# Optimization experiments

Hardware: AMD Instinct MI355X
Metric: run time of the kernel (lower is better)

The kernel has to match this reference:

```python
import jax, jax.numpy as jnp
import numpy as np

B, S, H, D = 4, 2048, 16, 64
DM = H * D  # d_model = 1024


def setup_inputs() -> dict:
    key = jax.random.key(0)
    ks = jax.random.split(key, 11)
    s = 1.0 / np.sqrt(DM)
    return {
        "query": jax.random.normal(ks[0], (B, S, DM), jnp.float32),
        "key": jax.random.normal(ks[1], (B, S, DM), jnp.float32),
        "value": jax.random.normal(ks[2], (B, S, DM), jnp.float32),
        "Wq": jax.random.uniform(ks[3], (DM, DM), jnp.float32, -s, s),
        "bq": jax.random.uniform(ks[4], (DM,), jnp.float32, -s, s),
        "Wk": jax.random.uniform(ks[5], (DM, DM), jnp.float32, -s, s),
        "bk": jax.random.uniform(ks[6], (DM,), jnp.float32, -s, s),
        "Wv": jax.random.uniform(ks[7], (DM, DM), jnp.float32, -s, s),
        "bv": jax.random.uniform(ks[8], (DM,), jnp.float32, -s, s),
        "Wo": jax.random.uniform(ks[9], (DM, DM), jnp.float32, -s, s),
        "bo": jax.random.uniform(ks[10], (DM,), jnp.float32, -s, s),
        "masking": 1,
    }


def reference(query, key, value, Wq, bq, Wk, bk, Wv, bv, Wo, bo, masking):
    b, s, _ = query.shape
    # Linear projections (torch Linear: x @ W.T + b), split into heads
    q = (query @ Wq.T + bq).reshape(b, s, H, D).transpose(0, 2, 1, 3)  # [B,H,S,D]
    k = (key @ Wk.T + bk).reshape(b, -1, H, D).transpose(0, 2, 1, 3)
    v = (value @ Wv.T + bv).reshape(b, -1, H, D).transpose(0, 2, 1, 3)
    scores = jnp.einsum("bhqd,bhkd->bhqk", q, k) / np.power(D, 0.5)
    if masking:
        # subsequent (strictly upper-triangular) mask -> fill with -1e9
        sub = jnp.triu(jnp.ones((s, k.shape[2]), bool), k=1)
        scores = jnp.where(sub, jnp.float32(-1e9), scores)
    attn = jax.nn.softmax(scores, axis=-1)
    out = jnp.einsum("bhqk,bhkd->bhqd", attn, v)  # [B,H,S,D]
    out = out.transpose(0, 2, 1, 3).reshape(b, s, H * D)
    return out @ Wo.T + bo
```

## Files before the change

kernel.cpp:

```cpp
#include <hip/hip_runtime.h>
#include <stdint.h>
#include <stddef.h>

#define B_ 4
#define S_ 2048
#define H_ 16
#define D_ 64
#define DM 1024
#define MTOT 8192
#define QSCALE 0.1803368867f

typedef __bf16 bf16x8 __attribute__((ext_vector_type(8)));
typedef __bf16 bf16x4 __attribute__((ext_vector_type(4)));
typedef float  f32x4  __attribute__((ext_vector_type(4)));

__device__ __forceinline__ void g2l16(const void* g, void* l) {
  __builtin_amdgcn_global_load_lds(
      (__attribute__((address_space(1))) void*)g,
      (__attribute__((address_space(3))) void*)l, 16, 0, 0);
}

__global__ __launch_bounds__(256) void cvt_kernel(const float* __restrict__ src,
                                                  __bf16* __restrict__ dst, int n4,
                                                  float scale) {
  int i = blockIdx.x * 256 + threadIdx.x;
  if (i < n4) {
    const float4 v = ((const float4*)src)[i];
    bf16x4 o;
    o.x = (__bf16)(v.x * scale); o.y = (__bf16)(v.y * scale);
    o.z = (__bf16)(v.z * scale); o.w = (__bf16)(v.w * scale);
    ((bf16x4*)dst)[i] = o;
  }
}

struct QKVArgs {
  const __bf16 *A0, *A1, *A2;
  const __bf16 *W0, *W1, *W2;
  const float *b0, *b1, *b2;
  __bf16 *oQ, *oK, *oVt;
};

__global__ __launch_bounds__(256) void gemm_qkv(QKVArgs args) {
  const int z = blockIdx.z;
  const __bf16* A    = (z == 0) ? args.A0 : (z == 1) ? args.A1 : args.A2;
  const __bf16* W    = (z == 0) ? args.W0 : (z == 1) ? args.W1 : args.W2;
  const float*  bias = (z == 0) ? args.b0 : (z == 1) ? args.b1 : args.b2;
  const float   bsc  = (z == 0) ? QSCALE : 1.0f;

  __shared__ __bf16 As[128 * 32];
  __shared__ __bf16 Bs[128 * 32];

  const int m0 = blockIdx.x * 128;
  const int n0 = blockIdx.y * 128;
  const int tid = threadIdx.x;
  const int wave = tid >> 6, lane = tid & 63;
  const int lrow = lane & 15, lhi = lane >> 4;
  const int moff = (wave & 1) * 64, noff = (wave >> 1) * 64;
  const int srow = lane >> 2;
  const int schunk = (lane & 3) * 8;

  f32x4 acc[4][4] = {};

  for (int k0 = 0; k0 < DM; k0 += 32) {
#pragma unroll
    for (int p = 0; p < 2; ++p) {
      const int rg = (p * 4 + wave) * 16;
      g2l16(A + (size_t)(m0 + rg + srow) * DM + k0 + schunk, As + rg * 32 + lane * 8);
      g2l16(W + (size_t)(n0 + rg + srow) * DM + k0 + schunk, Bs + rg * 32 + lane * 8);
    }
    __syncthreads();
    bf16x8 af[4], bfr[4];
#pragma unroll
    for (int i = 0; i < 4; ++i) {
      af[i]  = *(const bf16x8*)(As + (moff + i * 16 + lrow) * 32 + lhi * 8);
      bfr[i] = *(const bf16x8*)(Bs + (noff + i * 16 + lrow) * 32 + lhi * 8);
    }
#pragma unroll
    for (int i = 0; i < 4; ++i)
#pragma unroll
      for (int j = 0; j < 4; ++j)
        acc[i][j] = __builtin_amdgcn_mfma_f32_16x16x32_bf16(af[i], bfr[j], acc[i][j], 0, 0, 0);
    __syncthreads();
  }

  if (z < 2) {
    __bf16* out = (z == 0) ? args.oQ : args.oK;
#pragma unroll
    for (int i = 0; i < 4; ++i)
#pragma unroll
      for (int j = 0; j < 4; ++j)
#pragma unroll
        for (int r = 0; r < 4; ++r) {
          const int row = m0 + moff + i * 16 + lhi * 4 + r;
          const int col = n0 + noff + j * 16 + lrow;
          out[(size_t)row * DM + col] = (__bf16)(acc[i][j][r] + bias[col] * bsc);
        }
  } else {
    __bf16* out = args.oVt;
#pragma unroll
    for (int i = 0; i < 4; ++i)
#pragma unroll
      for (int j = 0; j < 4; ++j)
#pragma unroll
        for (int r = 0; r < 4; ++r) {
          const int row = m0 + moff + i * 16 + lhi * 4 + r;
          const int col = n0 + noff + j * 16 + lrow;
          const int bb = row >> 11, s = row & 2047;
          const int hh = col >> 6,  d = col & 63;
          out[(((size_t)(bb * H_ + hh) * D_ + d) << 11) + s] =
              (__bf16)(acc[i][j][r] + bias[col]);
        }
  }
}

__global__ __launch_bounds__(256) void gemm_oproj(const __bf16* __restrict__ A,
                                                  const __bf16* __restrict__ W,
                                                  const float* __restrict__ bias,
                                                  float* __restrict__ out) {
  __shared__ __bf16 As[128 * 32];
  __shared__ __bf16 Bs[128 * 32];

  const int m0 = blockIdx.x * 128;
  const int n0 = blockIdx.y * 128;
  const int tid = threadIdx.x;
  const int wave = tid >> 6, lane = tid & 63;
  const int lrow = lane & 15, lhi = lane >> 4;
  const int moff = (wave & 1) * 64, noff = (wave >> 1) * 64;
  const int srow = lane >> 2;
  const int schunk = (lane & 3) * 8;

  f32x4 acc[4][4] = {};

  for (int k0 = 0; k0 < DM; k0 += 32) {
#pragma unroll
    for (int p = 0; p < 2; ++p) {
      const int rg = (p * 4 + wave) * 16;
      g2l16(A + (size_t)(m0 + rg + srow) * DM + k0 + schunk, As + rg * 32 + lane * 8);
      g2l16(W + (size_t)(n0 + rg + srow) * DM + k0 + schunk, Bs + rg * 32 + lane * 8);
    }
    __syncthreads();
    bf16x8 af[4], bfr[4];
#pragma unroll
    for (int i = 0; i < 4; ++i) {
      af[i]  = *(const bf16x8*)(As + (moff + i * 16 + lrow) * 32 + lhi * 8);
      bfr[i] = *(const bf16x8*)(Bs + (noff + i * 16 + lrow) * 32 + lhi * 8);
    }
#pragma unroll
    for (int i = 0; i < 4; ++i)
#pragma unroll
      for (int j = 0; j < 4; ++j)
        acc[i][j] = __builtin_amdgcn_mfma_f32_16x16x32_bf16(af[i], bfr[j], acc[i][j], 0, 0, 0);
    __syncthreads();
  }

#pragma unroll
  for (int i = 0; i < 4; ++i)
#pragma unroll
    for (int j = 0; j < 4; ++j)
#pragma unroll
      for (int r = 0; r < 4; ++r) {
        const int row = m0 + moff + i * 16 + lhi * 4 + r;
        const int col = n0 + noff + j * 16 + lrow;
        out[(size_t)row * DM + col] = acc[i][j][r] + bias[col];
      }
}

__global__ __launch_bounds__(256, 3) void attn_kernel(const __bf16* __restrict__ Q,
                                                      const __bf16* __restrict__ K,
                                                      const __bf16* __restrict__ Vt,
                                                      __bf16* __restrict__ O) {
  const int id = blockIdx.x;
  const int slot = id >> 8;
  const int tau = id & 255;
  const int k4 = (tau >> 3) & 3;
  const int bh = ((tau >> 5) << 3) | (tau & 7);
  const int b = bh >> 4, h = bh & 15;

  int tiles[2];
  int ntile;
  if (slot == 0)      { ntile = 1; tiles[0] = 15 - k4; tiles[1] = 0; }
  else if (slot == 1) { ntile = 1; tiles[0] = 8 + k4;  tiles[1] = 0; }
  else                { ntile = 2; tiles[0] = k4;      tiles[1] = 7 - k4; }

  const int wave = threadIdx.x >> 6;
  const int lane = threadIdx.x & 63;
  const int lq = lane & 15, lhi = lane >> 4;

  const __bf16* Qb = Q + (size_t)b * S_ * DM + h * D_;
  const __bf16* Kb = K + (size_t)b * S_ * DM + h * D_;
  const __bf16* Vb = Vt + (size_t)bh * D_ * S_;

  __shared__ __bf16 Ks[2][64 * 64];
  __shared__ __bf16 Vs[2][64 * 64];
  __shared__ __bf16 Ps[4][32 * 72];
  __bf16* const Pw = Ps[wave];

  const int rl = lane >> 3;
  const int cg8 = ((lane & 7) ^ rl) * 8;

  for (int ti = 0; ti < ntile; ++ti) {
    const int t = tiles[ti];
    const int qw0 = t * 128 + wave * 32;
    const int jend = t * 128 + 64;

    if (ti) __syncthreads();

    bf16x8 qb[2][2];
#pragma unroll
    for (int m = 0; m < 2; ++m)
#pragma unroll
      for (int kd = 0; kd < 2; ++kd)
        qb[m][kd] = *(const bf16x8*)(Qb + (size_t)(qw0 + m * 16 + lq) * DM + kd * 32 + lhi * 8);

    f32x4 o_acc[2][4] = {};
    float rs[2] = {0.f, 0.f};

#pragma unroll
    for (int i = 0; i < 2; ++i) {
      const int row = wave * 16 + i * 8 + rl;
      g2l16(Kb + (size_t)row * DM + cg8, Ks[0] + ((wave * 16 + i * 8) << 6) + lane * 8);
      g2l16(Vb + (size_t)row * S_ + cg8, Vs[0] + ((wave * 16 + i * 8) << 6) + lane * 8);
    }

    int p = 0;
    for (int j0 = 0; j0 <= jend; j0 += 64) {
      __syncthreads();
      if (j0 < jend) {
        const int jn = j0 + 64;
#pragma unroll
        for (int i = 0; i < 2; ++i) {
          const int row = wave * 16 + i * 8 + rl;
          g2l16(Kb + (size_t)(jn + row) * DM + cg8, Ks[p ^ 1] + ((wave * 16 + i * 8) << 6) + lane * 8);
          g2l16(Vb + (size_t)row * S_ + jn + cg8, Vs[p ^ 1] + ((wave * 16 + i * 8) << 6) + lane * 8);
        }
      }

      bf16x8 kf[4][2];
#pragma unroll
      for (int kt = 0; kt < 4; ++kt) {
        const int r = kt * 16 + lq;
#pragma unroll
        for (int kd = 0; kd < 2; ++kd)
          kf[kt][kd] = *(const bf16x8*)(Ks[p] + (r << 6) + (((kd * 4 + lhi) ^ (r & 7)) << 3));
      }

      bf16x8 vf[4][2];
#pragma unroll
      for (int dt = 0; dt < 4; ++dt) {
        const int r = dt * 16 + lq;
#pragma unroll
        for (int kk = 0; kk < 2; ++kk)
          vf[dt][kk] = *(const bf16x8*)(Vs[p] + (r << 6) + (((kk * 4 + lhi) ^ (r & 7)) << 3));
      }

      f32x4 sc[2][4];
#pragma unroll
      for (int m = 0; m < 2; ++m)
#pragma unroll
        for (int kt = 0; kt < 4; ++kt) {
          f32x4 s = {};
          s = __builtin_amdgcn_mfma_f32_16x16x32_bf16(kf[kt][0], qb[m][0], s, 0, 0, 0);
          s = __builtin_amdgcn_mfma_f32_16x16x32_bf16(kf[kt][1], qb[m][1], s, 0, 0, 0);
          sc[m][kt] = s;
        }

#pragma unroll
      for (int m = 0; m < 2; ++m) {
        const bool dg = (j0 + 63 > qw0 + m * 16);
        const int thr = qw0 + m * 16 + lq - j0;
#pragma unroll
        for (int kt = 0; kt < 4; ++kt) {
          bf16x4 pk;
#pragma unroll
          for (int r = 0; r < 4; ++r) {
            float v = sc[m][kt][r];
            if (dg && (kt * 16 + lhi * 4 + r > thr)) v = -1e9f;
            const float pv = exp2f(v);
            rs[m] += pv;
            pk[r] = (__bf16)pv;
          }
          *(bf16x4*)(Pw + (m * 16 + lq) * 72 + kt * 16 + lhi * 4) = pk;
        }
      }

#pragma unroll
      for (int m = 0; m < 2; ++m) {
        bf16x8 pa[2];
#pragma unroll
        for (int kk = 0; kk < 2; ++kk)
          pa[kk] = *(const bf16x8*)(Pw + (m * 16 + lq) * 72 + kk * 32 + lhi * 8);
#pragma unroll
        for (int dt = 0; dt < 4; ++dt) {
          o_acc[m][dt] = __builtin_amdgcn_mfma_f32_16x16x32_bf16(pa[0], vf[dt][0], o_acc[m][dt], 0, 0, 0);
          o_acc[m][dt] = __builtin_amdgcn_mfma_f32_16x16x32_bf16(pa[1], vf[dt][1], o_acc[m][dt], 0, 0, 0);
        }
      }
      p ^= 1;
    }

#pragma unroll
    for (int m = 0; m < 2; ++m) {
      rs[m] += __shfl_xor(rs[m], 16);
      rs[m] += __shfl_xor(rs[m], 32);
    }

#pragma unroll
    for (int m = 0; m < 2; ++m)
#pragma unroll
      for (int r = 0; r < 4; ++r) {
        const float inv = 1.0f / __shfl(rs[m], lhi * 4 + r);
        const int qrow = qw0 + m * 16 + lhi * 4 + r;
        __bf16* orow = O + ((size_t)b * S_ + qrow) * DM + h * D_;
#pragma unroll
        for (int dt = 0; dt < 4; ++dt)
          orow[dt * 16 + lq] = (__bf16)(o_acc[m][dt][r] * inv);
      }
  }
}

extern "C" void kernel_launch(void* const* d_in, const int* in_sizes, int n_in,
                              void* d_out, int out_size, void* d_ws, size_t ws_size,
                              hipStream_t stream) {
  (void)in_sizes; (void)n_in; (void)out_size; (void)ws_size;
  const float* query = (const float*)d_in[0];
  const float* key   = (const float*)d_in[1];
  const float* value = (const float*)d_in[2];
  const float* Wq = (const float*)d_in[3];
  const float* bq = (const float*)d_in[4];
  const float* Wk = (const float*)d_in[5];
  const float* bk = (const float*)d_in[6];
  const float* Wv = (const float*)d_in[7];
  const float* bv = (const float*)d_in[8];
  const float* Wo = (const float*)d_in[9];
  const float* bo = (const float*)d_in[10];

  const size_t NX = (size_t)MTOT * DM;
  const size_t NW = (size_t)DM * DM;
  __bf16* p = (__bf16*)d_ws;
  __bf16 *Xq = p, *Xk = Xq + NX, *Xv = Xk + NX;
  __bf16 *Wqb = Xv + NX, *Wkb = Wqb + NW, *Wvb = Wkb + NW, *Wob = Wvb + NW;
  __bf16 *Qrm = Wob + NW, *Krm = Qrm + NX, *Vt = Krm + NX, *Orm = Vt + NX;

  const int nbx = (int)(NX / 4 / 256);
  const int nbw = (int)(NW / 4 / 256);
  cvt_kernel<<<nbx, 256, 0, stream>>>(query, Xq, (int)(NX / 4), 1.0f);
  cvt_kernel<<<nbx, 256, 0, stream>>>(key,   Xk, (int)(NX / 4), 1.0f);
  cvt_kernel<<<nbx, 256, 0, stream>>>(value, Xv, (int)(NX / 4), 1.0f);
  cvt_kernel<<<nbw, 256, 0, stream>>>(Wq, Wqb, (int)(NW / 4), QSCALE);
  cvt_kernel<<<nbw, 256, 0, stream>>>(Wk, Wkb, (int)(NW / 4), 1.0f);
  cvt_kernel<<<nbw, 256, 0, stream>>>(Wv, Wvb, (int)(NW / 4), 1.0f);
  cvt_kernel<<<nbw, 256, 0, stream>>>(Wo, Wob, (int)(NW / 4), 1.0f);

  QKVArgs qa;
  qa.A0 = Xq; qa.A1 = Xk; qa.A2 = Xv;
  qa.W0 = Wqb; qa.W1 = Wkb; qa.W2 = Wvb;
  qa.b0 = bq; qa.b1 = bk; qa.b2 = bv;
  qa.oQ = Qrm; qa.oK = Krm; qa.oVt = Vt;
  gemm_qkv<<<dim3(MTOT / 128, DM / 128, 3), 256, 0, stream>>>(qa);

  attn_kernel<<<dim3(768), 256, 0, stream>>>(Qrm, Krm, Vt, Orm);

  gemm_oproj<<<dim3(MTOT / 128, DM / 128), 256, 0, stream>>>(Orm, Wob, bo, (float*)d_out);
}
```

Before: 345.1 us.

## Pipeline GEMMs with triple-buffered swizzled LDS, 256x128 tiles, and fuse conversions

Replaces the simple single-buffer GEMM loop in the QKV and output projections with a shared main loop. It uses 256x128 tiles, a triple-buffered LDS ring filled by global_load_lds, XOR-swizzled LDS addressing to avoid bank conflicts, and MFMA phases interleaved with prefetches under raised wave priority. The aim is to hide global-load latency behind compute and raise data reuse per tile. The seven fp32-to-bf16 conversion launches are also merged into one launch to cut launch overhead. The cost is more registers and LDS per block (occupancy 2), plus hand-tuned waitcnt logic that is fragile.

```diff
diff --git a/kernel.cpp b/kernel.cpp
--- a/kernel.cpp
+++ b/kernel.cpp
@@ -20,17 +20,124 @@
       (__attribute__((address_space(3))) void*)l, 16, 0, 0);
 }
 
-__global__ __launch_bounds__(256) void cvt_kernel(const float* __restrict__ src,
-                                                  __bf16* __restrict__ dst, int n4,
-                                                  float scale) {
-  int i = blockIdx.x * 256 + threadIdx.x;
-  if (i < n4) {
-    const float4 v = ((const float4*)src)[i];
-    bf16x4 o;
-    o.x = (__bf16)(v.x * scale); o.y = (__bf16)(v.y * scale);
-    o.z = (__bf16)(v.z * scale); o.w = (__bf16)(v.w * scale);
-    ((bf16x4*)dst)[i] = o;
+struct Cvt7 {
+  const float* s[7];
+  __bf16* d[7];
+  float sc[7];
+};
+__global__ __launch_bounds__(256) void cvt_all(Cvt7 a) {
+  const int b = blockIdx.x;
+  int seg, i;
+  if (b < 24576) { seg = b >> 13; i = ((b & 8191) << 8) + threadIdx.x; }
+  else { const int sb = b - 24576; seg = 3 + (sb >> 10); i = ((sb & 1023) << 8) + threadIdx.x; }
+  const float sc = a.sc[seg];
+  const float4 v = ((const float4*)a.s[seg])[i];
+  bf16x4 o;
+  o.x = (__bf16)(v.x * sc); o.y = (__bf16)(v.y * sc);
+  o.z = (__bf16)(v.z * sc); o.w = (__bf16)(v.w * sc);
+  ((bf16x4*)a.d[seg])[i] = o;
+}
+
+__device__ __forceinline__ void gemm_main(const __bf16* __restrict__ A,
+                                          const __bf16* __restrict__ W,
+                                          int m0, int n0,
+                                          __bf16* ldsA, __bf16* ldsB,
+                                          f32x4 (&acc)[8][4]) {
+  const int tid = threadIdx.x;
+  const int lane = tid & 63, wave = tid >> 6;
+  const int lq = lane & 15, lhi = lane >> 4;
+  const int wr = wave >> 1, wc = wave & 1;
+
+  const int srow = tid >> 2;
+  const int cso = ((tid & 3) ^ (srow & 3)) * 8;
+  const __bf16* pA = A + (size_t)(m0 + srow) * DM + cso;
+  const __bf16* pB = W + (size_t)(n0 + srow) * DM + cso;
+  const int tid8 = tid * 8;
+
+  const int sx = (lhi ^ (lq & 3)) * 8;
+  const int aB = (wr * 128 + lq) * 32 + sx;
+  const int bB = (wc * 64 + lq) * 32 + sx;
+
+#define SA(q, ko, bs) g2l16(pA + (size_t)(q) * 64 * DM + (ko), ldsA + (bs) * 8192 + (q) * 2048 + tid8)
+#define SB(q, ko, bs) g2l16(pB + (size_t)(q) * 64 * DM + (ko), ldsB + (bs) * 4096 + (q) * 2048 + tid8)
+
+  SA(0, 0, 0); SA(1, 0, 0); SA(2, 0, 0); SA(3, 0, 0); SB(0, 0, 0); SB(1, 0, 0);
+  SA(0, 32, 1); SA(1, 32, 1); SA(2, 32, 1); SA(3, 32, 1); SB(0, 32, 1); SB(1, 32, 1);
+  asm volatile("s_waitcnt vmcnt(6)" ::: "memory");
+  __builtin_amdgcn_s_barrier();
+  __builtin_amdgcn_sched_barrier(0);
+
+  int bR = 0, bN = 1, bS = 2;
+  int koS = 64;
+#pragma unroll 1
+  for (int t = 0; t < 32; ++t) {
+    const __bf16* lA = ldsA + bR * 8192;
+    const __bf16* lB = ldsB + bR * 4096;
+    const bool s2 = t < 30;
+    bf16x8 af[8], bf[4];
+
+#pragma unroll
+    for (int m = 0; m < 4; ++m) af[m] = *(const bf16x8*)(lA + aB + m * 512);
+#pragma unroll
+    for (int n = 0; n < 2; ++n) bf[n] = *(const bf16x8*)(lB + bB + n * 512);
+    if (s2) { SA(0, koS, bS); SA(1, koS, bS); }
+    __builtin_amdgcn_s_barrier();
+    __builtin_amdgcn_sched_barrier(0);
+    __builtin_amdgcn_s_setprio(1);
+#pragma unroll
+    for (int m = 0; m < 4; ++m)
+#pragma unroll
+      for (int n = 0; n < 2; ++n)
+        acc[m][n] = __builtin_amdgcn_mfma_f32_16x16x32_bf16(af[m], bf[n], acc[m][n], 0, 0, 0);
+    __builtin_amdgcn_s_setprio(0);
+
+#pragma unroll
+    for (int m = 4; m < 8; ++m) af[m] = *(const bf16x8*)(lA + aB + m * 512);
+    if (s2) { SA(2, koS, bS); SA(3, koS, bS); }
+    __builtin_amdgcn_s_barrier();
+    __builtin_amdgcn_sched_barrier(0);
+    __builtin_amdgcn_s_setprio(1);
+#pragma unroll
+    for (int m = 4; m < 8; ++m)
+#pragma unroll
+      for (int n = 0; n < 2; ++n)
+        acc[m][n] = __builtin_amdgcn_mfma_f32_16x16x32_bf16(af[m], bf[n], acc[m][n], 0, 0, 0);
+    __builtin_amdgcn_s_setprio(0);
+
+#pragma unroll
+    for (int n = 2; n < 4; ++n) bf[n] = *(const bf16x8*)(lB + bB + n * 512);
+    if (s2) SB(0, koS, bS);
+    __builtin_amdgcn_s_barrier();
+    __builtin_amdgcn_sched_barrier(0);
+    __builtin_amdgcn_s_setprio(1);
+#pragma unroll
+    for (int m = 0; m < 4; ++m)
+#pragma unroll
+      for (int n = 2; n < 4; ++n)
+        acc[m][n] = __builtin_amdgcn_mfma_f32_16x16x32_bf16(af[m], bf[n], acc[m][n], 0, 0, 0);
+    __builtin_amdgcn_s_setprio(0);
+
+    if (s2) SB(1, koS, bS);
+    if (t < 30) {
+      asm volatile("s_waitcnt vmcnt(6)" ::: "memory");
+    } else if (t == 30) {
+      asm volatile("s_waitcnt vmcnt(0)" ::: "memory");
+    }
+    __builtin_amdgcn_s_barrier();
+    __builtin_amdgcn_sched_barrier(0);
+    __builtin_amdgcn_s_setprio(1);
+#pragma unroll
+    for (int m = 4; m < 8; ++m)
+#pragma unroll
+      for (int n = 2; n < 4; ++n)
+        acc[m][n] = __builtin_amdgcn_mfma_f32_16x16x32_bf16(af[m], bf[n], acc[m][n], 0, 0, 0);
+    __builtin_amdgcn_s_setprio(0);
+
+    const int x = bR; bR = bN; bN = bS; bS = x;
+    koS += 32;
   }
+#undef SA
+#undef SB
 }
 
 struct QKVArgs {
@@ -40,128 +147,82 @@
   __bf16 *oQ, *oK, *oVt;
 };
 
-__global__ __launch_bounds__(256) void gemm_qkv(QKVArgs args) {
+__global__ __launch_bounds__(256, 2) void gemm_qkv(QKVArgs args) {
   const int z = blockIdx.z;
   const __bf16* A    = (z == 0) ? args.A0 : (z == 1) ? args.A1 : args.A2;
   const __bf16* W    = (z == 0) ? args.W0 : (z == 1) ? args.W1 : args.W2;
   const float*  bias = (z == 0) ? args.b0 : (z == 1) ? args.b1 : args.b2;
   const float   bsc  = (z == 0) ? QSCALE : 1.0f;
 
-  __shared__ __bf16 As[128 * 32];
-  __shared__ __bf16 Bs[128 * 32];
-
-  const int m0 = blockIdx.x * 128;
+  __shared__ __bf16 ldsA[3 * 8192];
+  __shared__ __bf16 ldsB[3 * 4096];
+
+  const int m0 = blockIdx.x * 256;
   const int n0 = blockIdx.y * 128;
-  const int tid = threadIdx.x;
-  const int wave = tid >> 6, lane = tid & 63;
-  const int lrow = lane & 15, lhi = lane >> 4;
-  const int moff = (wave & 1) * 64, noff = (wave >> 1) * 64;
-  const int srow = lane >> 2;
-  const int schunk = (lane & 3) * 8;
-
-  f32x4 acc[4][4] = {};
-
-  for (int k0 = 0; k0 < DM; k0 += 32) {
-#pragma unroll
-    for (int p = 0; p < 2; ++p) {
-      const int rg = (p * 4 + wave) * 16;
-      g2l16(A + (size_t)(m0 + rg + srow) * DM + k0 + schunk, As + rg * 32 + lane * 8);
-      g2l16(W + (size_t)(n0 + rg + srow) * DM + k0 + schunk, Bs + rg * 32 + lane * 8);
-    }
-    __syncthreads();
-    bf16x8 af[4], bfr[4];
-#pragma unroll
-    for (int i = 0; i < 4; ++i) {
-      af[i]  = *(const bf16x8*)(As + (moff + i * 16 + lrow) * 32 + lhi * 8);
-      bfr[i] = *(const bf16x8*)(Bs + (noff + i * 16 + lrow) * 32 + lhi * 8);
-    }
-#pragma unroll
-    for (int i = 0; i < 4; ++i)
-#pragma unroll
-      for (int j = 0; j < 4; ++j)
-        acc[i][j] = __builtin_amdgcn_mfma_f32_16x16x32_bf16(af[i], bfr[j], acc[i][j], 0, 0, 0);
-    __syncthreads();
-  }
+
+  f32x4 acc[8][4] = {};
+  gemm_main(A, W, m0, n0, ldsA, ldsB, acc);
+
+  const int lane = threadIdx.x & 63, wave = threadIdx.x >> 6;
+  const int lq = lane & 15, lhi = lane >> 4;
+  const int wr = wave >> 1, wc = wave & 1;
 
   if (z < 2) {
     __bf16* out = (z == 0) ? args.oQ : args.oK;
 #pragma unroll
-    for (int i = 0; i < 4; ++i)
-#pragma unroll
-      for (int j = 0; j < 4; ++j)
+    for (int m = 0; m < 8; ++m)
+#pragma unroll
+      for (int n = 0; n < 4; ++n)
 #pragma unroll
         for (int r = 0; r < 4; ++r) {
-          const int row = m0 + moff + i * 16 + lhi * 4 + r;
-          const int col = n0 + noff + j * 16 + lrow;
-          out[(size_t)row * DM + col] = (__bf16)(acc[i][j][r] + bias[col] * bsc);
+          const int row = m0 + wr * 128 + m * 16 + lhi * 4 + r;
+          const int col = n0 + wc * 64 + n * 16 + lq;
+          out[(size_t)row * DM + col] = (__bf16)(acc[m][n][r] + bias[col] * bsc);
         }
   } else {
     __bf16* out = args.oVt;
 #pragma unroll
-    for (int i = 0; i < 4; ++i)
-#pragma unroll
-      for (int j = 0; j < 4; ++j)
+    for (int m = 0; m < 8; ++m)
+#pragma unroll
+      for (int n = 0; n < 4; ++n)
 #pragma unroll
         for (int r = 0; r < 4; ++r) {
-          const int row = m0 + moff + i * 16 + lhi * 4 + r;
-          const int col = n0 + noff + j * 16 + lrow;
+          const int row = m0 + wr * 128 + m * 16 + lhi * 4 + r;
+          const int col = n0 + wc * 64 + n * 16 + lq;
           const int bb = row >> 11, s = row & 2047;
           const int hh = col >> 6,  d = col & 63;
           out[(((size_t)(bb * H_ + hh) * D_ + d) << 11) + s] =
-              (__bf16)(acc[i][j][r] + bias[col]);
+              (__bf16)(acc[m][n][r] + bias[col]);
         }
   }
 }
 
-__global__ __launch_bounds__(256) void gemm_oproj(const __bf16* __restrict__ A,
-                                                  const __bf16* __restrict__ W,
-                                                  const float* __restrict__ bias,
-                                                  float* __restrict__ out) {
-  __shared__ __bf16 As[128 * 32];
-  __shared__ __bf16 Bs[128 * 32];
-
-  const int m0 = blockIdx.x * 128;
+__global__ __launch_bounds__(256, 2) void gemm_oproj(const __bf16* __restrict__ A,
+                                                     const __bf16* __restrict__ W,
+                                                     const float* __restrict__ bias,
+                                                     float* __restrict__ out) {
+  __shared__ __bf16 ldsA[3 * 8192];
+  __shared__ __bf16 ldsB[3 * 4096];
+
+  const int m0 = blockIdx.x * 256;
   const int n0 = blockIdx.y * 128;
-  const int tid = threadIdx.x;
-  const int wave = tid >> 6, lane = tid & 63;
-  const int lrow = lane & 15, lhi = lane >> 4;
-  const int moff = (wave & 1) * 64, noff = (wave >> 1) * 64;
-  const int srow = lane >> 2;
-  const int schunk = (lane & 3) * 8;
-
-  f32x4 acc[4][4] = {};
-
-  for (int k0 = 0; k0 < DM; k0 += 32) {
-#pragma unroll
-    for (int p = 0; p < 2; ++p) {
-      const int rg = (p * 4 + wave) * 16;
-      g2l16(A + (size_t)(m0 + rg + srow) * DM + k0 + schunk, As + rg * 32 + lane * 8);
-      g2l16(W + (size_t)(n0 + rg + srow) * DM + k0 + schunk, Bs + rg * 32 + lane * 8);
-    }
-    __syncthreads();
-    bf16x8 af[4], bfr[4];
-#pragma unroll
-    for (int i = 0; i < 4; ++i) {
-      af[i]  = *(const bf16x8*)(As + (moff + i * 16 + lrow) * 32 + lhi * 8);
-      bfr[i] = *(const bf16x8*)(Bs + (noff + i * 16 + lrow) * 32 + lhi * 8);
-    }
-#pragma unroll
-    for (int i = 0; i < 4; ++i)
-#pragma unroll
-      for (int j = 0; j < 4; ++j)
-        acc[i][j] = __builtin_amdgcn_mfma_f32_16x16x32_bf16(af[i], bfr[j], acc[i][j], 0, 0, 0);
-    __syncthreads();
-  }
-
-#pragma unroll
-  for (int i = 0; i < 4; ++i)
-#pragma unroll
-    for (int j = 0; j < 4; ++j)
+
+  f32x4 acc[8][4] = {};
+  gemm_main(A, W, m0, n0, ldsA, ldsB, acc);
+
+  const int lane = threadIdx.x & 63, wave = threadIdx.x >> 6;
+  const int lq = lane & 15, lhi = lane >> 4;
+  const int wr = wave >> 1, wc = wave & 1;
+
+#pragma unroll
+  for (int m = 0; m < 8; ++m)
+#pragma unroll
+    for (int n = 0; n < 4; ++n)
 #pragma unroll
       for (int r = 0; r < 4; ++r) {
-        const int row = m0 + moff + i * 16 + lhi * 4 + r;
-        const int col = n0 + noff + j * 16 + lrow;
-        out[(size_t)row * DM + col] = acc[i][j][r] + bias[col];
+        const int row = m0 + wr * 128 + m * 16 + lhi * 4 + r;
+        const int col = n0 + wc * 64 + n * 16 + lq;
+        out[(size_t)row * DM + col] = acc[m][n][r] + bias[col];
       }
 }
 
@@ -341,24 +402,24 @@
   __bf16 *Wqb = Xv + NX, *Wkb = Wqb + NW, *Wvb = Wkb + NW, *Wob = Wvb + NW;
   __bf16 *Qrm = Wob + NW, *Krm = Qrm + NX, *Vt = Krm + NX, *Orm = Vt + NX;
 
-  const int nbx = (int)(NX / 4 / 256);
-  const int nbw = (int)(NW / 4 / 256);
-  cvt_kernel<<<nbx, 256, 0, stream>>>(query, Xq, (int)(NX / 4), 1.0f);
-  cvt_kernel<<<nbx, 256, 0, stream>>>(key,   Xk, (int)(NX / 4), 1.0f);
-  cvt_kernel<<<nbx, 256, 0, stream>>>(value, Xv, (int)(NX / 4), 1.0f);
-  cvt_kernel<<<nbw, 256, 0, stream>>>(Wq, Wqb, (int)(NW / 4), QSCALE);
-  cvt_kernel<<<nbw, 256, 0, stream>>>(Wk, Wkb, (int)(NW / 4), 1.0f);
-  cvt_kernel<<<nbw, 256, 0, stream>>>(Wv, Wvb, (int)(NW / 4), 1.0f);
-  cvt_kernel<<<nbw, 256, 0, stream>>>(Wo, Wob, (int)(NW / 4), 1.0f);
+  Cvt7 ca;
+  ca.s[0] = query; ca.s[1] = key; ca.s[2] = value;
+  ca.s[3] = Wq; ca.s[4] = Wk; ca.s[5] = Wv; ca.s[6] = Wo;
+  ca.d[0] = Xq; ca.d[1] = Xk; ca.d[2] = Xv;
+  ca.d[3] = Wqb; ca.d[4] = Wkb; ca.d[5] = Wvb; ca.d[6] = Wob;
+  ca.sc[0] = 1.0f; ca.sc[1] = 1.0f; ca.sc[2] = 1.0f;
+  ca.sc[3] = QSCALE;
+  ca.sc[4] = 1.0f; ca.sc[5] = 1.0f; ca.sc[6] = 1.0f;
+  cvt_all<<<28672, 256, 0, stream>>>(ca);
 
   QKVArgs qa;
   qa.A0 = Xq; qa.A1 = Xk; qa.A2 = Xv;
   qa.W0 = Wqb; qa.W1 = Wkb; qa.W2 = Wvb;
   qa.b0 = bq; qa.b1 = bk; qa.b2 = bv;
   qa.oQ = Qrm; qa.oK = Krm; qa.oVt = Vt;
-  gemm_qkv<<<dim3(MTOT / 128, DM / 128, 3), 256, 0, stream>>>(qa);
+  gemm_qkv<<<dim3(MTOT / 256, DM / 128, 3), 256, 0, stream>>>(qa);
 
   attn_kernel<<<dim3(768), 256, 0, stream>>>(Qrm, Krm, Vt, Orm);
 
-  gemm_oproj<<<dim3(MTOT / 128, DM / 128), 256, 0, stream>>>(Orm, Wob, bo, (float*)d_out);
-}
+  gemm_oproj<<<dim3(MTOT / 256, DM / 128), 256, 0, stream>>>(Orm, Wob, bo, (float*)d_out);
+}
```

Measured after the change: 332.4 us. 1.04x faster.
